# Performance work log

Hardware: AMD Instinct MI355X
Metric: run time of the kernel (lower is better)

## Reference

```python
import jax, jax.numpy as jnp
import numpy as np

V = 200000   # total vertices
K = 96       # neighbours per vertex (incl. self)
NSEG = 4     # number of row-split segments


def setup_inputs() -> dict:
    key = jax.random.key(0)
    k1, k2 = jax.random.split(key)
    seg_size = V // NSEG
    row_splits = (jnp.arange(NSEG + 1, dtype=jnp.int32) * seg_size)
    seg_id = jnp.repeat(jnp.arange(NSEG, dtype=jnp.int32), seg_size)
    seg_start = row_splits[seg_id]                      # (V,)
    # segment-local random neighbours, self index in column 0 (kNN convention)
    offs = jax.random.randint(k1, (V, K), 0, seg_size, dtype=jnp.int32)
    neighs = seg_start[:, None] + offs
    neighs = neighs.at[:, 0].set(jnp.arange(V, dtype=jnp.int32))
    hier = jax.random.uniform(k2, (V, 1), dtype=jnp.float32)
    return {"neighs": neighs, "hier": hier, "row_splits": row_splits}


def _cluster(neighs, hier, row_splits):
    """Greedy hierarchy-ordered neighbour clustering (NMS-like).

    Returns:
      sel     (V,1) int32: cluster-centre vertex indices, compacted to the
              front in processing order, padded with -1 (original op returns
              a dynamically sized tensor; we pad for fixed shapes).
      rs      (n_seg+1,) int32: row splits after selection.
      ggather (V,1) int32: for each vertex, the position in `sel` of its
              cluster centre (gather-back indices).
    """
    Vn, _ = neighs.shape
    n_seg = row_splits.shape[0] - 1
    seg_id = jnp.searchsorted(row_splits[1:], jnp.arange(Vn), side='right').astype(jnp.int32)
    # per-segment argsort descending on hier, with global offsets == global
    # lexsort by (segment, -hier) since vertices are segment-contiguous
    order = jnp.lexsort((-hier[:, 0], seg_id)).astype(jnp.int32)  # (V,)

    def step(assign, v):
        is_new = assign[v] < 0                 # v not yet absorbed -> new centre
        nb = neighs[v]                          # (K,) neighbour indices
        grab = is_new & (assign[nb] < 0)        # unassigned neighbours get taken
        assign = assign.at[jnp.where(is_new, v, Vn)].set(v, mode='drop')
        assign = assign.at[jnp.where(grab, nb, Vn)].set(v, mode='drop')
        return assign, is_new

    assign0 = jnp.full((Vn,), -1, jnp.int32)
    assign, is_new = jax.lax.scan(step, assign0, order)  # assign: centre vertex per vertex

    new_i = is_new.astype(jnp.int32)
    pos = jnp.cumsum(new_i) - 1                           # rank of each centre in order
    sel = jnp.full((Vn,), -1, jnp.int32).at[jnp.where(is_new, pos, Vn)].set(order, mode='drop')
    counts = jax.ops.segment_sum(new_i, seg_id[order], num_segments=n_seg)
    rs = jnp.concatenate([jnp.zeros((1,), jnp.int32), jnp.cumsum(counts).astype(jnp.int32)])
    center_rank = jnp.zeros((Vn,), jnp.int32).at[jnp.where(is_new, order, Vn)].set(pos, mode='drop')
    ggather = center_rank[assign].reshape(-1, 1)
    return sel.reshape(-1, 1), rs, ggather


def reference(neighs, hier, row_splits):
    return _cluster(neighs, hier, row_splits)
```

## Files before the change

### kernel.cpp

```cpp
#include <hip/hip_runtime.h>
#include <hip/hip_cooperative_groups.h>

namespace cg = cooperative_groups;

#define IDX_BITS 20
#define IDX_MASK ((1u << IDX_BITS) - 1)
#define NT1 1024
#define MAX_G1 512
#define T1 49152
#define TB2 16
#define T2 1536
#define GRID_ROUND_CAP 16
#define MAX_ROUNDS 8000
#define SC_CAP 1024
#define SV_CAP 4096

typedef unsigned long long u64;

__device__ __forceinline__ u64 pack_key(float h, int v) {
  return ((u64)(~__float_as_uint(h)) << IDX_BITS) | (unsigned)v;
}

struct Ctx {
  const int* __restrict__ neighs;
  const float* __restrict__ hier;
  const int* __restrict__ row_splits;
  int V, K, nseg;
  u64* assign;
  int* tag;
  int* listA;
  int* listB;
  u64* centre_key;
  int* centre_v;
  int* rank_of;
  int* cnt;
  int* out_sel;
  int* out_rs;
  int* out_gg;
};

struct BlkState {
  int sc_cnt, sv_cnt, sc_base, sv_base;
  int seg_hist[8];
  int sc_list[SC_CAP];
  int sv_list[SV_CAP];
};

__device__ __forceinline__ void xbar(int* bar, int target) {
  __syncthreads();
  __threadfence();
  if (threadIdx.x == 0) {
    __hip_atomic_fetch_add(bar, 1, __ATOMIC_RELEASE, __HIP_MEMORY_SCOPE_AGENT);
    while (__hip_atomic_load(bar, __ATOMIC_ACQUIRE, __HIP_MEMORY_SCOPE_AGENT) < target)
      __builtin_amdgcn_s_sleep(2);
  }
  __syncthreads();
  __threadfence();
}

__device__ __forceinline__ void record_direct(const Ctx& c, int v, u64 pv) {
  int slot = atomicAdd(&c.cnt[2], 1);
  int seg = 0;
  for (int t = 1; t < c.nseg; ++t) seg += (v >= c.row_splits[t]);
  c.centre_v[slot] = v;
  c.centre_key[slot] = ((u64)seg << 52) | pv;
  atomicAdd(&c.cnt[8 + seg], 1);
}

__device__ __forceinline__ void phaseB(const Ctx& c, const int* rl, int an, int r,
                                       int qs, int qst, int ql) {
  if (c.K == 96) {
    for (int i = qs; i < an; i += qst) {
      int u = rl ? rl[i] : i;
      u64 pu = pack_key(c.hier[u], u);
      if (c.assign[u] <= pu) continue;
      const int* row = c.neighs + (size_t)u * 96;
      int w[6];
#pragma unroll
      for (int t = 0; t < 6; ++t) w[t] = row[ql + 16 * t];
#pragma unroll
      for (int t = 0; t < 6; ++t)
        if (pack_key(c.hier[w[t]], w[t]) > pu) c.tag[w[t]] = r;
    }
  } else {
    for (int i = qs; i < an; i += qst) {
      int u = rl ? rl[i] : i;
      u64 pu = pack_key(c.hier[u], u);
      if (c.assign[u] <= pu) continue;
      const int* row = c.neighs + (size_t)u * c.K;
      for (int j = ql; j < c.K; j += 16) {
        int w = row[j];
        if (pack_key(c.hier[w], w) > pu) c.tag[w] = r;
      }
    }
  }
}

__device__ __forceinline__ void phaseC(const Ctx& c, BlkState& bs, const int* rl,
                                       int* wl, int* survc, int an, int r,
                                       int qs, int qst, int ql) {
  for (int i = qs; i < an; i += qst) {
    int u = rl ? rl[i] : i;
    u64 pu = pack_key(c.hier[u], u);
    if (c.assign[u] <= pu) continue;
    if (c.tag[u] != r) {
      const int* row = c.neighs + (size_t)u * c.K;
      for (int j = ql; j < c.K; j += 16) atomicMin(&c.assign[row[j]], pu);
      if (ql == 0) {
        int s = atomicAdd(&bs.sc_cnt, 1);
        if (s < SC_CAP) bs.sc_list[s] = u; else record_direct(c, u, pu);
      }
    } else if (ql == 0) {
      u64 y = __hip_atomic_load(&c.assign[u], __ATOMIC_RELAXED, __HIP_MEMORY_SCOPE_AGENT);
      if (y > pu) {
        int s = atomicAdd(&bs.sv_cnt, 1);
        if (s < SV_CAP) bs.sv_list[s] = u;
        else { int g = atomicAdd(survc, 1); wl[g] = u; }
      }
    }
  }
}

__device__ __forceinline__ void flush_block(const Ctx& c, BlkState& bs, int* wl, int* survc) {
  __syncthreads();
  int nsc = min(bs.sc_cnt, SC_CAP), nsv = min(bs.sv_cnt, SV_CAP);
  if (threadIdx.x == 0 && nsc) bs.sc_base = atomicAdd(&c.cnt[2], nsc);
  if (threadIdx.x == 0 && nsv) bs.sv_base = atomicAdd(survc, nsv);
  if (threadIdx.x < 8) bs.seg_hist[threadIdx.x] = 0;
  __syncthreads();
  for (int i = threadIdx.x; i < nsv; i += blockDim.x) wl[bs.sv_base + i] = bs.sv_list[i];
  for (int i = threadIdx.x; i < nsc; i += blockDim.x) {
    int v = bs.sc_list[i];
    int seg = 0;
    for (int t = 1; t < c.nseg; ++t) seg += (v >= c.row_splits[t]);
    c.centre_v[bs.sc_base + i] = v;
    c.centre_key[bs.sc_base + i] = ((u64)seg << 52) | pack_key(c.hier[v], v);
    atomicAdd(&bs.seg_hist[seg], 1);
  }
  __syncthreads();
  if (threadIdx.x < c.nseg) {
    int h = bs.seg_hist[threadIdx.x];
    if (h) atomicAdd(&c.cnt[8 + threadIdx.x], h);
  }
  __syncthreads();
  if (threadIdx.x == 0) { bs.sc_cnt = 0; bs.sv_cnt = 0; }
}

__global__ void __launch_bounds__(NT1) k_tier1(Ctx c) {
  cg::grid_group grid = cg::this_grid();
  __shared__ BlkState bs;
  const int tid = blockIdx.x * blockDim.x + threadIdx.x;
  const int nthr = gridDim.x * blockDim.x;
  const int ql = threadIdx.x & 15;
  const int qg = tid >> 4, nq = nthr >> 4;
  if (threadIdx.x == 0) { bs.sc_cnt = 0; bs.sv_cnt = 0; }
  __syncthreads();

  int aliveN = c.V, r = 0;
  while (true) {
    const int* rl = (r & 1) ? c.listA : c.listB;
    int* wl = (r & 1) ? c.listB : c.listA;
    if (tid == 0) c.cnt[(r + 1) & 1] = 0;
    phaseB(c, r ? rl : nullptr, aliveN, r, qg, nq, ql);
    __threadfence();
    grid.sync();
    phaseC(c, bs, r ? rl : nullptr, wl, &c.cnt[(r + 1) & 1], aliveN, r, qg, nq, ql);
    flush_block(c, bs, wl, &c.cnt[(r + 1) & 1]);
    __threadfence();
    grid.sync();
    aliveN = c.cnt[(r + 1) & 1];
    ++r;
    if (aliveN == 0 || aliveN <= T1 || r >= GRID_ROUND_CAP) break;
  }
  if (tid == 0) { c.cnt[5] = aliveN; c.cnt[6] = r; }
}

__global__ void __launch_bounds__(NT1) k_tail(Ctx c) {
  __shared__ BlkState bs;
  const int ql = threadIdx.x & 15;
  const int bq = threadIdx.x >> 4;
  const int NBQ = NT1 >> 4;
  const int trank = blockIdx.x;
  if (threadIdx.x == 0) { bs.sc_cnt = 0; bs.sv_cnt = 0; }
  __syncthreads();

  int an = c.cnt[5], tr = c.cnt[6];

  if (an > T2) {
    const int qstart = trank * NBQ + bq;
    const int qstride = TB2 * NBQ;
    int ep = 0;
    while (true) {
      const int* rl = (tr & 1) ? c.listA : c.listB;
      int* wl = (tr & 1) ? c.listB : c.listA;
      if (trank == 0 && threadIdx.x == 0) c.cnt[(tr + 1) & 1] = 0;
      phaseB(c, rl, an, tr, qstart, qstride, ql);
      xbar(&c.cnt[3], TB2 * (++ep));
      phaseC(c, bs, rl, wl, &c.cnt[(tr + 1) & 1], an, tr, qstart, qstride, ql);
      flush_block(c, bs, wl, &c.cnt[(tr + 1) & 1]);
      xbar(&c.cnt[3], TB2 * (++ep));
      an = c.cnt[(tr + 1) & 1];
      ++tr;
      if (an == 0 || an <= T2 || tr >= MAX_ROUNDS) break;
    }
  }
  if (trank != 0) return;

  while (an > 0 && tr < MAX_ROUNDS) {
    const int* rl = (tr & 1) ? c.listA : c.listB;
    int* wl = (tr & 1) ? c.listB : c.listA;
    if (threadIdx.x == 0) c.cnt[(tr + 1) & 1] = 0;
    phaseB(c, rl, an, tr, bq, NBQ, ql);
    __threadfence(); __syncthreads();
    phaseC(c, bs, rl, wl, &c.cnt[(tr + 1) & 1], an, tr, bq, NBQ, ql);
    flush_block(c, bs, wl, &c.cnt[(tr + 1) & 1]);
    __threadfence(); __syncthreads();
    an = c.cnt[(tr + 1) & 1];
    ++tr;
  }
}

__global__ void __launch_bounds__(NT1) k_rank(Ctx c) {
  __shared__ u64 shp[NT1];
  const int nC = c.cnt[2];
  for (int base = blockIdx.x * NT1; base < nC; base += gridDim.x * NT1) {
    int idx = base + threadIdx.x;
    bool have = idx < nC;
    u64 mykey = have ? c.centre_key[idx] : 0;
    int myv = have ? c.centre_v[idx] : 0;
    int myrank = 0;
    for (int cs = 0; cs < nC; cs += NT1) {
      int j = cs + threadIdx.x;
      shp[threadIdx.x] = (j < nC) ? c.centre_key[j] : ~0ull;
      __syncthreads();
      int lim = min(NT1, nC - cs);
      for (int t = 0; t < lim; ++t) myrank += (shp[t] < mykey) ? 1 : 0;
      __syncthreads();
    }
    if (have) {
      c.out_sel[myrank] = myv;
      c.rank_of[myv] = myrank;
    }
  }
  if (blockIdx.x == 0 && threadIdx.x == 0) {
    int run = 0;
    c.out_rs[0] = 0;
    for (int s = 0; s < c.nseg; ++s) { run += c.cnt[8 + s]; c.out_rs[s + 1] = run; }
  }
}

__global__ void __launch_bounds__(256) k_gg(Ctx c) {
  int v = blockIdx.x * blockDim.x + threadIdx.x;
  const int stride = gridDim.x * blockDim.x;
  for (; v < c.V; v += stride) {
    u64 y = c.assign[v];
    u64 pv = pack_key(c.hier[v], v);
    int ctr = (y < pv) ? (int)(y & IDX_MASK) : v;
    c.out_gg[v] = c.rank_of[ctr];
  }
}

extern "C" void kernel_launch(void* const* d_in, const int* in_sizes, int n_in,
                              void* d_out, int out_size, void* d_ws, size_t ws_size,
                              hipStream_t stream) {
  Ctx c;
  c.neighs = (const int*)d_in[0];
  c.hier = (const float*)d_in[1];
  c.row_splits = (const int*)d_in[2];
  c.V = in_sizes[1];
  c.K = in_sizes[0] / c.V;
  c.nseg = in_sizes[2] - 1;

  char* pm = (char*)d_ws;
  const size_t V = (size_t)c.V;
  c.assign = (u64*)pm;        pm += V * 8;
  c.tag = (int*)pm;           pm += V * 4;
  size_t ff_bytes = V * 12;
  c.listA = (int*)pm;         pm += V * 4;
  c.listB = (int*)pm;         pm += V * 4;
  c.centre_key = (u64*)pm;    pm += V * 8;
  c.centre_v = (int*)pm;      pm += V * 4;
  c.rank_of = (int*)pm;       pm += V * 4;
  c.cnt = (int*)pm;           pm += 64 * 4;

  int* out = (int*)d_out;
  c.out_sel = out;
  c.out_rs = out + c.V;
  c.out_gg = out + c.V + c.nseg + 1;

  hipMemsetAsync(d_ws, 0xFF, ff_bytes, stream);
  hipMemsetAsync((void*)c.cnt, 0, 64 * 4, stream);
  hipMemsetAsync((void*)c.out_sel, 0xFF, V * 4, stream);

  int dev = 0, nCU = 0, maxB = 0;
  hipGetDevice(&dev);
  hipDeviceGetAttribute(&nCU, hipDeviceAttributeMultiprocessorCount, dev);
  hipOccupancyMaxActiveBlocksPerMultiprocessor(&maxB, k_tier1, NT1, 0);
  if (nCU <= 0) nCU = 256;
  if (maxB <= 0) maxB = 1;
  int g1 = nCU * maxB;
  if (g1 > MAX_G1) g1 = MAX_G1;

  void* args[] = { &c };
  hipLaunchCooperativeKernel((void*)k_tier1, dim3(g1), dim3(NT1), args, 0, stream);
  k_tail<<<TB2, NT1, 0, stream>>>(c);
  k_rank<<<16, NT1, 0, stream>>>(c);
  k_gg<<<512, 256, 0, stream>>>(c);
}
```

Measured before the change: 2.028 ms.

## Fuse tag and claim phases into one pass per round with lagged tags

Merges the separate tag (phaseB) and claim (phaseC) passes into a single fused pass per round, so each round needs one grid barrier instead of two. Tags written in round r are checked against a threshold of r-2, which lets the tagging of one round overlap the claiming of the next. A precomputed per-vertex byte mask of higher-priority neighbours (kmask) removes the repeated hier gathers from later tagging. Round counters rotate over four slots, and the cooperative grid.sync is replaced by a custom atomic barrier. The lagged tags may be less precise, which could add rounds, and kmask costs V*16 bytes of workspace.

Result: slower. 2.254 ms (+11.2%).

```diff
diff --git a/kernel.cpp b/kernel.cpp
--- a/kernel.cpp
+++ b/kernel.cpp
@@ -1,7 +1,4 @@
 #include <hip/hip_runtime.h>
-#include <hip/hip_cooperative_groups.h>
-
-namespace cg = cooperative_groups;
 
 #define IDX_BITS 20
 #define IDX_MASK ((1u << IDX_BITS) - 1)
@@ -33,6 +30,7 @@
   u64* centre_key;
   int* centre_v;
   int* rank_of;
+  unsigned char* kmask;
   int* cnt;
   int* out_sel;
   int* out_rs;
@@ -59,7 +57,7 @@
 }
 
 __device__ __forceinline__ void record_direct(const Ctx& c, int v, u64 pv) {
-  int slot = atomicAdd(&c.cnt[2], 1);
+  int slot = atomicAdd(&c.cnt[4], 1);
   int seg = 0;
   for (int t = 1; t < c.nseg; ++t) seg += (v >= c.row_splits[t]);
   c.centre_v[slot] = v;
@@ -67,64 +65,110 @@
   atomicAdd(&c.cnt[8 + seg], 1);
 }
 
-__device__ __forceinline__ void phaseB(const Ctx& c, const int* rl, int an, int r,
-                                       int qs, int qst, int ql) {
+__device__ __forceinline__ void round0_tag(const Ctx& c, int qs, int qst, int ql) {
+  if (c.K == 96) {
+    for (int i = qs; i < c.V; i += qst) {
+      int u = i;
+      u64 pu = pack_key(c.hier[u], u);
+      const int* row = c.neighs + (size_t)u * 96;
+      int w[6];
+#pragma unroll
+      for (int t = 0; t < 6; ++t) w[t] = row[ql + 16 * t];
+      unsigned m = 0;
+#pragma unroll
+      for (int t = 0; t < 6; ++t) {
+        if (pack_key(c.hier[w[t]], w[t]) > pu) { m |= (1u << t); c.tag[w[t]] = 0; }
+      }
+      c.kmask[(size_t)u * 16 + ql] = (unsigned char)m;
+    }
+  } else {
+    for (int i = qs; i < c.V; i += qst) {
+      int u = i;
+      u64 pu = pack_key(c.hier[u], u);
+      const int* row = c.neighs + (size_t)u * c.K;
+      for (int j = ql; j < c.K; j += 16) {
+        int w = row[j];
+        if (pack_key(c.hier[w], w) > pu) c.tag[w] = 0;
+      }
+    }
+  }
+}
+
+__device__ __forceinline__ void fused_pass(const Ctx& c, BlkState& bs, const int* rl,
+                                           int* wl, int* survc, int an, int r, int thr,
+                                           bool dotag, int qs, int qst, int ql) {
   if (c.K == 96) {
     for (int i = qs; i < an; i += qst) {
       int u = rl ? rl[i] : i;
       u64 pu = pack_key(c.hier[u], u);
-      if (c.assign[u] <= pu) continue;
-      const int* row = c.neighs + (size_t)u * 96;
-      int w[6];
-#pragma unroll
-      for (int t = 0; t < 6; ++t) w[t] = row[ql + 16 * t];
-#pragma unroll
-      for (int t = 0; t < 6; ++t)
-        if (pack_key(c.hier[w[t]], w[t]) > pu) c.tag[w[t]] = r;
+      u64 y = c.assign[u];
+      if (y <= pu) continue;
+      if (c.tag[u] <= thr) {
+        const int* row = c.neighs + (size_t)u * 96;
+#pragma unroll
+        for (int t = 0; t < 6; ++t) atomicMin(&c.assign[row[ql + 16 * t]], pu);
+        if (ql == 0) {
+          int s = atomicAdd(&bs.sc_cnt, 1);
+          if (s < SC_CAP) bs.sc_list[s] = u; else record_direct(c, u, pu);
+        }
+      } else {
+        if (dotag) {
+          const int* row = c.neighs + (size_t)u * 96;
+          unsigned m = c.kmask[(size_t)u * 16 + ql];
+          int w[6];
+#pragma unroll
+          for (int t = 0; t < 6; ++t) w[t] = row[ql + 16 * t];
+#pragma unroll
+          for (int t = 0; t < 6; ++t)
+            if (m & (1u << t)) c.tag[w[t]] = r;
+        }
+        if (ql == 0) {
+          u64 yf = __hip_atomic_load(&c.assign[u], __ATOMIC_RELAXED, __HIP_MEMORY_SCOPE_AGENT);
+          if (yf > pu) {
+            int s = atomicAdd(&bs.sv_cnt, 1);
+            if (s < SV_CAP) bs.sv_list[s] = u;
+            else { int g = atomicAdd(survc, 1); wl[g] = u; }
+          }
+        }
+      }
     }
   } else {
     for (int i = qs; i < an; i += qst) {
       int u = rl ? rl[i] : i;
       u64 pu = pack_key(c.hier[u], u);
-      if (c.assign[u] <= pu) continue;
+      u64 y = c.assign[u];
+      if (y <= pu) continue;
       const int* row = c.neighs + (size_t)u * c.K;
-      for (int j = ql; j < c.K; j += 16) {
-        int w = row[j];
-        if (pack_key(c.hier[w], w) > pu) c.tag[w] = r;
+      if (c.tag[u] <= thr) {
+        for (int j = ql; j < c.K; j += 16) atomicMin(&c.assign[row[j]], pu);
+        if (ql == 0) {
+          int s = atomicAdd(&bs.sc_cnt, 1);
+          if (s < SC_CAP) bs.sc_list[s] = u; else record_direct(c, u, pu);
+        }
+      } else {
+        if (dotag) {
+          for (int j = ql; j < c.K; j += 16) {
+            int w = row[j];
+            if (pack_key(c.hier[w], w) > pu) c.tag[w] = r;
+          }
+        }
+        if (ql == 0) {
+          u64 yf = __hip_atomic_load(&c.assign[u], __ATOMIC_RELAXED, __HIP_MEMORY_SCOPE_AGENT);
+          if (yf > pu) {
+            int s = atomicAdd(&bs.sv_cnt, 1);
+            if (s < SV_CAP) bs.sv_list[s] = u;
+            else { int g = atomicAdd(survc, 1); wl[g] = u; }
+          }
+        }
       }
     }
   }
 }
 
-__device__ __forceinline__ void phaseC(const Ctx& c, BlkState& bs, const int* rl,
-                                       int* wl, int* survc, int an, int r,
-                                       int qs, int qst, int ql) {
-  for (int i = qs; i < an; i += qst) {
-    int u = rl ? rl[i] : i;
-    u64 pu = pack_key(c.hier[u], u);
-    if (c.assign[u] <= pu) continue;
-    if (c.tag[u] != r) {
-      const int* row = c.neighs + (size_t)u * c.K;
-      for (int j = ql; j < c.K; j += 16) atomicMin(&c.assign[row[j]], pu);
-      if (ql == 0) {
-        int s = atomicAdd(&bs.sc_cnt, 1);
-        if (s < SC_CAP) bs.sc_list[s] = u; else record_direct(c, u, pu);
-      }
-    } else if (ql == 0) {
-      u64 y = __hip_atomic_load(&c.assign[u], __ATOMIC_RELAXED, __HIP_MEMORY_SCOPE_AGENT);
-      if (y > pu) {
-        int s = atomicAdd(&bs.sv_cnt, 1);
-        if (s < SV_CAP) bs.sv_list[s] = u;
-        else { int g = atomicAdd(survc, 1); wl[g] = u; }
-      }
-    }
-  }
-}
-
 __device__ __forceinline__ void flush_block(const Ctx& c, BlkState& bs, int* wl, int* survc) {
   __syncthreads();
   int nsc = min(bs.sc_cnt, SC_CAP), nsv = min(bs.sv_cnt, SV_CAP);
-  if (threadIdx.x == 0 && nsc) bs.sc_base = atomicAdd(&c.cnt[2], nsc);
+  if (threadIdx.x == 0 && nsc) bs.sc_base = atomicAdd(&c.cnt[4], nsc);
   if (threadIdx.x == 0 && nsv) bs.sv_base = atomicAdd(survc, nsv);
   if (threadIdx.x < 8) bs.seg_hist[threadIdx.x] = 0;
   __syncthreads();
@@ -147,30 +191,34 @@
 }
 
 __global__ void __launch_bounds__(NT1) k_tier1(Ctx c) {
-  cg::grid_group grid = cg::this_grid();
   __shared__ BlkState bs;
   const int tid = blockIdx.x * blockDim.x + threadIdx.x;
   const int nthr = gridDim.x * blockDim.x;
   const int ql = threadIdx.x & 15;
   const int qg = tid >> 4, nq = nthr >> 4;
+  const int nb = gridDim.x;
   if (threadIdx.x == 0) { bs.sc_cnt = 0; bs.sv_cnt = 0; }
   __syncthreads();
 
-  int aliveN = c.V, r = 0;
-  while (true) {
+  int ep = 0;
+  round0_tag(c, qg, nq, ql);
+  xbar(&c.cnt[16], nb * (++ep));
+  if (tid == 0) c.cnt[1] = 0;
+  fused_pass(c, bs, nullptr, c.listA, &c.cnt[0], c.V, 0, -1, false, qg, nq, ql);
+  flush_block(c, bs, c.listA, &c.cnt[0]);
+  xbar(&c.cnt[16], nb * (++ep));
+
+  int aliveN = c.cnt[0];
+  int r = 1;
+  while (aliveN > T1 && r <= GRID_ROUND_CAP) {
     const int* rl = (r & 1) ? c.listA : c.listB;
     int* wl = (r & 1) ? c.listB : c.listA;
-    if (tid == 0) c.cnt[(r + 1) & 1] = 0;
-    phaseB(c, r ? rl : nullptr, aliveN, r, qg, nq, ql);
-    __threadfence();
-    grid.sync();
-    phaseC(c, bs, r ? rl : nullptr, wl, &c.cnt[(r + 1) & 1], aliveN, r, qg, nq, ql);
-    flush_block(c, bs, wl, &c.cnt[(r + 1) & 1]);
-    __threadfence();
-    grid.sync();
-    aliveN = c.cnt[(r + 1) & 1];
+    if (tid == 0) c.cnt[(r + 1) & 3] = 0;
+    fused_pass(c, bs, rl, wl, &c.cnt[r & 3], aliveN, r, r - 2, true, qg, nq, ql);
+    flush_block(c, bs, wl, &c.cnt[r & 3]);
+    xbar(&c.cnt[16], nb * (++ep));
+    aliveN = c.cnt[r & 3];
     ++r;
-    if (aliveN == 0 || aliveN <= T1 || r >= GRID_ROUND_CAP) break;
   }
   if (tid == 0) { c.cnt[5] = aliveN; c.cnt[6] = r; }
 }
@@ -190,18 +238,15 @@
     const int qstart = trank * NBQ + bq;
     const int qstride = TB2 * NBQ;
     int ep = 0;
-    while (true) {
+    while (an > T2 && tr < MAX_ROUNDS) {
       const int* rl = (tr & 1) ? c.listA : c.listB;
       int* wl = (tr & 1) ? c.listB : c.listA;
-      if (trank == 0 && threadIdx.x == 0) c.cnt[(tr + 1) & 1] = 0;
-      phaseB(c, rl, an, tr, qstart, qstride, ql);
-      xbar(&c.cnt[3], TB2 * (++ep));
-      phaseC(c, bs, rl, wl, &c.cnt[(tr + 1) & 1], an, tr, qstart, qstride, ql);
-      flush_block(c, bs, wl, &c.cnt[(tr + 1) & 1]);
-      xbar(&c.cnt[3], TB2 * (++ep));
-      an = c.cnt[(tr + 1) & 1];
+      if (trank == 0 && threadIdx.x == 0) c.cnt[(tr + 1) & 3] = 0;
+      fused_pass(c, bs, rl, wl, &c.cnt[tr & 3], an, tr, tr - 2, true, qstart, qstride, ql);
+      flush_block(c, bs, wl, &c.cnt[tr & 3]);
+      xbar(&c.cnt[32], TB2 * (++ep));
+      an = c.cnt[tr & 3];
       ++tr;
-      if (an == 0 || an <= T2 || tr >= MAX_ROUNDS) break;
     }
   }
   if (trank != 0) return;
@@ -209,20 +254,18 @@
   while (an > 0 && tr < MAX_ROUNDS) {
     const int* rl = (tr & 1) ? c.listA : c.listB;
     int* wl = (tr & 1) ? c.listB : c.listA;
-    if (threadIdx.x == 0) c.cnt[(tr + 1) & 1] = 0;
-    phaseB(c, rl, an, tr, bq, NBQ, ql);
+    if (threadIdx.x == 0) c.cnt[(tr + 1) & 3] = 0;
+    fused_pass(c, bs, rl, wl, &c.cnt[tr & 3], an, tr, tr - 2, true, bq, NBQ, ql);
+    flush_block(c, bs, wl, &c.cnt[tr & 3]);
     __threadfence(); __syncthreads();
-    phaseC(c, bs, rl, wl, &c.cnt[(tr + 1) & 1], an, tr, bq, NBQ, ql);
-    flush_block(c, bs, wl, &c.cnt[(tr + 1) & 1]);
-    __threadfence(); __syncthreads();
-    an = c.cnt[(tr + 1) & 1];
+    an = c.cnt[tr & 3];
     ++tr;
   }
 }
 
 __global__ void __launch_bounds__(NT1) k_rank(Ctx c) {
   __shared__ u64 shp[NT1];
-  const int nC = c.cnt[2];
+  const int nC = c.cnt[4];
   for (int base = blockIdx.x * NT1; base < nC; base += gridDim.x * NT1) {
     int idx = base + threadIdx.x;
     bool have = idx < nC;
@@ -281,6 +324,7 @@
   c.centre_key = (u64*)pm;    pm += V * 8;
   c.centre_v = (int*)pm;      pm += V * 4;
   c.rank_of = (int*)pm;       pm += V * 4;
+  c.kmask = (unsigned char*)pm; pm += V * 16;
   c.cnt = (int*)pm;           pm += 64 * 4;
 
   int* out = (int*)d_out;
```

## Replace grid.sync and fences with relaxed-atomic barriers, split tail into two kernels

Applied to the files above, without the earlier changes.

Removes the cooperative-groups grid.sync and the __threadfence calls. A custom atomic counter barrier with relaxed ordering takes their place, and shared data is read and written with relaxed agent-scope atomic loads and stores so the fences are not needed. The old tail kernel is split into a 16-block tier2 kernel and a single-block tier3 kernel. Round 0 no longer reads assign in phaseB, and the K=96 atomicMin loop is unrolled. Dropping the release/acquire ordering risks memory-ordering bugs, since correctness now depends on relaxed atomics bypassing non-coherent caches.

After: 1.625 ms. -19.9%, faster.

```diff
diff --git a/kernel.cpp b/kernel.cpp
--- a/kernel.cpp
+++ b/kernel.cpp
@@ -1,7 +1,4 @@
 #include <hip/hip_runtime.h>
-#include <hip/hip_cooperative_groups.h>
-
-namespace cg = cooperative_groups;
 
 #define IDX_BITS 20
 #define IDX_MASK ((1u << IDX_BITS) - 1)
@@ -19,6 +16,16 @@
 
 __device__ __forceinline__ u64 pack_key(float h, int v) {
   return ((u64)(~__float_as_uint(h)) << IDX_BITS) | (unsigned)v;
+}
+
+__device__ __forceinline__ int ald(const int* p) {
+  return __hip_atomic_load((int*)p, __ATOMIC_RELAXED, __HIP_MEMORY_SCOPE_AGENT);
+}
+__device__ __forceinline__ u64 ald64(const u64* p) {
+  return __hip_atomic_load((u64*)p, __ATOMIC_RELAXED, __HIP_MEMORY_SCOPE_AGENT);
+}
+__device__ __forceinline__ void ast(int* p, int v) {
+  __hip_atomic_store(p, v, __ATOMIC_RELAXED, __HIP_MEMORY_SCOPE_AGENT);
 }
 
 struct Ctx {
@@ -48,18 +55,16 @@
 
 __device__ __forceinline__ void xbar(int* bar, int target) {
   __syncthreads();
-  __threadfence();
   if (threadIdx.x == 0) {
-    __hip_atomic_fetch_add(bar, 1, __ATOMIC_RELEASE, __HIP_MEMORY_SCOPE_AGENT);
-    while (__hip_atomic_load(bar, __ATOMIC_ACQUIRE, __HIP_MEMORY_SCOPE_AGENT) < target)
+    __hip_atomic_fetch_add(bar, 1, __ATOMIC_RELAXED, __HIP_MEMORY_SCOPE_AGENT);
+    while (__hip_atomic_load(bar, __ATOMIC_RELAXED, __HIP_MEMORY_SCOPE_AGENT) < target)
       __builtin_amdgcn_s_sleep(2);
   }
   __syncthreads();
-  __threadfence();
 }
 
 __device__ __forceinline__ void record_direct(const Ctx& c, int v, u64 pv) {
-  int slot = atomicAdd(&c.cnt[2], 1);
+  int slot = atomicAdd(&c.cnt[4], 1);
   int seg = 0;
   for (int t = 1; t < c.nseg; ++t) seg += (v >= c.row_splits[t]);
   c.centre_v[slot] = v;
@@ -71,26 +76,26 @@
                                        int qs, int qst, int ql) {
   if (c.K == 96) {
     for (int i = qs; i < an; i += qst) {
-      int u = rl ? rl[i] : i;
+      int u = rl ? ald(&rl[i]) : i;
       u64 pu = pack_key(c.hier[u], u);
-      if (c.assign[u] <= pu) continue;
+      if (rl && ald64(&c.assign[u]) <= pu) continue;
       const int* row = c.neighs + (size_t)u * 96;
       int w[6];
 #pragma unroll
       for (int t = 0; t < 6; ++t) w[t] = row[ql + 16 * t];
 #pragma unroll
       for (int t = 0; t < 6; ++t)
-        if (pack_key(c.hier[w[t]], w[t]) > pu) c.tag[w[t]] = r;
+        if (pack_key(c.hier[w[t]], w[t]) > pu) ast(&c.tag[w[t]], r);
     }
   } else {
     for (int i = qs; i < an; i += qst) {
-      int u = rl ? rl[i] : i;
+      int u = rl ? ald(&rl[i]) : i;
       u64 pu = pack_key(c.hier[u], u);
-      if (c.assign[u] <= pu) continue;
+      if (rl && ald64(&c.assign[u]) <= pu) continue;
       const int* row = c.neighs + (size_t)u * c.K;
       for (int j = ql; j < c.K; j += 16) {
         int w = row[j];
-        if (pack_key(c.hier[w], w) > pu) c.tag[w] = r;
+        if (pack_key(c.hier[w], w) > pu) ast(&c.tag[w], r);
       }
     }
   }
@@ -100,22 +105,27 @@
                                        int* wl, int* survc, int an, int r,
                                        int qs, int qst, int ql) {
   for (int i = qs; i < an; i += qst) {
-    int u = rl ? rl[i] : i;
+    int u = rl ? ald(&rl[i]) : i;
     u64 pu = pack_key(c.hier[u], u);
-    if (c.assign[u] <= pu) continue;
-    if (c.tag[u] != r) {
+    if (ald64(&c.assign[u]) <= pu) continue;
+    if (ald(&c.tag[u]) != r) {
       const int* row = c.neighs + (size_t)u * c.K;
-      for (int j = ql; j < c.K; j += 16) atomicMin(&c.assign[row[j]], pu);
+      if (c.K == 96) {
+#pragma unroll
+        for (int t = 0; t < 6; ++t) atomicMin(&c.assign[row[ql + 16 * t]], pu);
+      } else {
+        for (int j = ql; j < c.K; j += 16) atomicMin(&c.assign[row[j]], pu);
+      }
       if (ql == 0) {
         int s = atomicAdd(&bs.sc_cnt, 1);
         if (s < SC_CAP) bs.sc_list[s] = u; else record_direct(c, u, pu);
       }
     } else if (ql == 0) {
-      u64 y = __hip_atomic_load(&c.assign[u], __ATOMIC_RELAXED, __HIP_MEMORY_SCOPE_AGENT);
+      u64 y = ald64(&c.assign[u]);
       if (y > pu) {
         int s = atomicAdd(&bs.sv_cnt, 1);
         if (s < SV_CAP) bs.sv_list[s] = u;
-        else { int g = atomicAdd(survc, 1); wl[g] = u; }
+        else { int g = atomicAdd(survc, 1); ast(&wl[g], u); }
       }
     }
   }
@@ -124,11 +134,11 @@
 __device__ __forceinline__ void flush_block(const Ctx& c, BlkState& bs, int* wl, int* survc) {
   __syncthreads();
   int nsc = min(bs.sc_cnt, SC_CAP), nsv = min(bs.sv_cnt, SV_CAP);
-  if (threadIdx.x == 0 && nsc) bs.sc_base = atomicAdd(&c.cnt[2], nsc);
+  if (threadIdx.x == 0 && nsc) bs.sc_base = atomicAdd(&c.cnt[4], nsc);
   if (threadIdx.x == 0 && nsv) bs.sv_base = atomicAdd(survc, nsv);
   if (threadIdx.x < 8) bs.seg_hist[threadIdx.x] = 0;
   __syncthreads();
-  for (int i = threadIdx.x; i < nsv; i += blockDim.x) wl[bs.sv_base + i] = bs.sv_list[i];
+  for (int i = threadIdx.x; i < nsv; i += blockDim.x) ast(&wl[bs.sv_base + i], bs.sv_list[i]);
   for (int i = threadIdx.x; i < nsc; i += blockDim.x) {
     int v = bs.sc_list[i];
     int seg = 0;
@@ -147,82 +157,87 @@
 }
 
 __global__ void __launch_bounds__(NT1) k_tier1(Ctx c) {
-  cg::grid_group grid = cg::this_grid();
   __shared__ BlkState bs;
   const int tid = blockIdx.x * blockDim.x + threadIdx.x;
   const int nthr = gridDim.x * blockDim.x;
   const int ql = threadIdx.x & 15;
   const int qg = tid >> 4, nq = nthr >> 4;
+  const int nb = gridDim.x;
   if (threadIdx.x == 0) { bs.sc_cnt = 0; bs.sv_cnt = 0; }
   __syncthreads();
 
-  int aliveN = c.V, r = 0;
+  int aliveN = c.V, r = 0, ep = 0;
   while (true) {
     const int* rl = (r & 1) ? c.listA : c.listB;
     int* wl = (r & 1) ? c.listB : c.listA;
-    if (tid == 0) c.cnt[(r + 1) & 1] = 0;
+    if (tid == 0) ast(&c.cnt[(r + 1) & 1], 0);
     phaseB(c, r ? rl : nullptr, aliveN, r, qg, nq, ql);
-    __threadfence();
-    grid.sync();
+    xbar(&c.cnt[16], nb * (++ep));
     phaseC(c, bs, r ? rl : nullptr, wl, &c.cnt[(r + 1) & 1], aliveN, r, qg, nq, ql);
     flush_block(c, bs, wl, &c.cnt[(r + 1) & 1]);
-    __threadfence();
-    grid.sync();
-    aliveN = c.cnt[(r + 1) & 1];
+    xbar(&c.cnt[16], nb * (++ep));
+    aliveN = ald(&c.cnt[(r + 1) & 1]);
     ++r;
     if (aliveN == 0 || aliveN <= T1 || r >= GRID_ROUND_CAP) break;
   }
-  if (tid == 0) { c.cnt[5] = aliveN; c.cnt[6] = r; }
-}
-
-__global__ void __launch_bounds__(NT1) k_tail(Ctx c) {
+  if (tid == 0) { ast(&c.cnt[5], aliveN); ast(&c.cnt[6], r); }
+}
+
+__global__ void __launch_bounds__(NT1) k_tier2(Ctx c) {
+  __shared__ BlkState bs;
+  const int ql = threadIdx.x & 15;
+  const int NBQ = NT1 >> 4;
+  if (threadIdx.x == 0) { bs.sc_cnt = 0; bs.sv_cnt = 0; }
+  __syncthreads();
+
+  int an = ald(&c.cnt[5]), tr = ald(&c.cnt[6]);
+  if (an <= T2) return;
+
+  const int qstart = blockIdx.x * NBQ + (threadIdx.x >> 4);
+  const int qstride = TB2 * NBQ;
+  int ep = 0;
+  while (true) {
+    const int* rl = (tr & 1) ? c.listA : c.listB;
+    int* wl = (tr & 1) ? c.listB : c.listA;
+    if (blockIdx.x == 0 && threadIdx.x == 0) ast(&c.cnt[(tr + 1) & 1], 0);
+    phaseB(c, rl, an, tr, qstart, qstride, ql);
+    xbar(&c.cnt[32], TB2 * (++ep));
+    phaseC(c, bs, rl, wl, &c.cnt[(tr + 1) & 1], an, tr, qstart, qstride, ql);
+    flush_block(c, bs, wl, &c.cnt[(tr + 1) & 1]);
+    xbar(&c.cnt[32], TB2 * (++ep));
+    an = ald(&c.cnt[(tr + 1) & 1]);
+    ++tr;
+    if (an == 0 || an <= T2 || tr >= MAX_ROUNDS) break;
+  }
+  if (blockIdx.x == 0 && threadIdx.x == 0) { ast(&c.cnt[5], an); ast(&c.cnt[6], tr); }
+}
+
+__global__ void __launch_bounds__(NT1) k_tier3(Ctx c) {
   __shared__ BlkState bs;
   const int ql = threadIdx.x & 15;
   const int bq = threadIdx.x >> 4;
   const int NBQ = NT1 >> 4;
-  const int trank = blockIdx.x;
   if (threadIdx.x == 0) { bs.sc_cnt = 0; bs.sv_cnt = 0; }
   __syncthreads();
 
-  int an = c.cnt[5], tr = c.cnt[6];
-
-  if (an > T2) {
-    const int qstart = trank * NBQ + bq;
-    const int qstride = TB2 * NBQ;
-    int ep = 0;
-    while (true) {
-      const int* rl = (tr & 1) ? c.listA : c.listB;
-      int* wl = (tr & 1) ? c.listB : c.listA;
-      if (trank == 0 && threadIdx.x == 0) c.cnt[(tr + 1) & 1] = 0;
-      phaseB(c, rl, an, tr, qstart, qstride, ql);
-      xbar(&c.cnt[3], TB2 * (++ep));
-      phaseC(c, bs, rl, wl, &c.cnt[(tr + 1) & 1], an, tr, qstart, qstride, ql);
-      flush_block(c, bs, wl, &c.cnt[(tr + 1) & 1]);
-      xbar(&c.cnt[3], TB2 * (++ep));
-      an = c.cnt[(tr + 1) & 1];
-      ++tr;
-      if (an == 0 || an <= T2 || tr >= MAX_ROUNDS) break;
-    }
-  }
-  if (trank != 0) return;
-
+  int an = ald(&c.cnt[5]), tr = ald(&c.cnt[6]);
   while (an > 0 && tr < MAX_ROUNDS) {
     const int* rl = (tr & 1) ? c.listA : c.listB;
     int* wl = (tr & 1) ? c.listB : c.listA;
-    if (threadIdx.x == 0) c.cnt[(tr + 1) & 1] = 0;
+    if (threadIdx.x == 0) ast(&c.cnt[(tr + 1) & 1], 0);
     phaseB(c, rl, an, tr, bq, NBQ, ql);
-    __threadfence(); __syncthreads();
+    __syncthreads();
     phaseC(c, bs, rl, wl, &c.cnt[(tr + 1) & 1], an, tr, bq, NBQ, ql);
     flush_block(c, bs, wl, &c.cnt[(tr + 1) & 1]);
-    __threadfence(); __syncthreads();
-    an = c.cnt[(tr + 1) & 1];
+    __syncthreads();
+    an = ald(&c.cnt[(tr + 1) & 1]);
     ++tr;
   }
 }
 
 __global__ void __launch_bounds__(NT1) k_rank(Ctx c) {
   __shared__ u64 shp[NT1];
-  const int nC = c.cnt[2];
+  const int nC = c.cnt[4];
   for (int base = blockIdx.x * NT1; base < nC; base += gridDim.x * NT1) {
     int idx = base + threadIdx.x;
     bool have = idx < nC;
@@ -303,7 +318,8 @@
 
   void* args[] = { &c };
   hipLaunchCooperativeKernel((void*)k_tier1, dim3(g1), dim3(NT1), args, 0, stream);
-  k_tail<<<TB2, NT1, 0, stream>>>(c);
+  k_tier2<<<TB2, NT1, 0, stream>>>(c);
+  k_tier3<<<1, NT1, 0, stream>>>(c);
   k_rank<<<16, NT1, 0, stream>>>(c);
   k_gg<<<512, 256, 0, stream>>>(c);
 }
```
